# Kernel tuning notes

Hardware: AMD Instinct MI355X
Metric: run time of the kernel (lower is better)

The kernel has to match this reference:

```python
import jax, jax.numpy as jnp
import numpy as np

B = 64
L_IN = 4001
L_CONV = 998  # (4001-10)//4 + 1
D = 1000
EPS = 1e-5


def _convlin(x, cw, cb, lw, lb):
    # x: (B,1,4001), cw: (1,1,10), lw: (1000,998)
    y = jax.lax.conv_general_dilated(
        x, cw, window_strides=(4,), padding='VALID',
        dimension_numbers=('NCH', 'OIH', 'NCH')) + cb[None, :, None]  # (B,1,998)
    y = y @ lw.T + lb  # (B,1,1000)
    return jax.nn.relu(y)


def setup_inputs() -> dict:
    key = jax.random.key(0)
    ks = jax.random.split(key, 24)
    f32 = jnp.float32
    inp = {
        'x': jax.random.normal(ks[0], (B, 1, L_IN), dtype=f32),
        'bn_gamma': jnp.ones((L_IN,), f32),
        'bn_beta': jnp.zeros((L_IN,), f32),
        'bn_mean': jax.random.normal(ks[1], (L_IN,), f32) * 0.1,
        'bn_var': jax.random.uniform(ks[2], (L_IN,), f32, 0.5, 1.5),
        'conv_w_q': jax.random.normal(ks[3], (1, 1, 10), f32) * 0.3,
        'conv_b_q': jax.random.normal(ks[4], (1,), f32) * 0.1,
        'lin_w_q': jax.random.normal(ks[5], (D, L_CONV), f32) * (1.0 / np.sqrt(L_CONV)),
        'lin_b_q': jax.random.normal(ks[6], (D,), f32) * 0.02,
        'conv_w_k': jax.random.normal(ks[7], (1, 1, 10), f32) * 0.3,
        'conv_b_k': jax.random.normal(ks[8], (1,), f32) * 0.1,
        'lin_w_k': jax.random.normal(ks[9], (D, L_CONV), f32) * (1.0 / np.sqrt(L_CONV)),
        'lin_b_k': jax.random.normal(ks[10], (D,), f32) * 0.02,
        'conv_w_v': jax.random.normal(ks[11], (1, 1, 10), f32) * 0.3,
        'conv_b_v': jax.random.normal(ks[12], (1,), f32) * 0.1,
        'lin_w_v': jax.random.normal(ks[13], (D, L_CONV), f32) * (1.0 / np.sqrt(L_CONV)),
        'lin_b_v': jax.random.normal(ks[14], (D,), f32) * 0.02,
        'in_proj_w': jax.random.normal(ks[15], (3, 1), f32),
        'in_proj_b': jax.random.normal(ks[16], (3,), f32) * 0.02,
        'out_proj_w': jax.random.normal(ks[17], (1, 1), f32),
        'out_proj_b': jax.random.normal(ks[18], (1,), f32) * 0.02,
        'out_w': jax.random.normal(ks[19], (D, D), f32) * (1.0 / np.sqrt(D)),
        'out_b': jax.random.normal(ks[20], (D,), f32) * 0.02,
    }
    return inp


def reference(x, bn_gamma, bn_beta, bn_mean, bn_var,
              conv_w_q, conv_b_q, lin_w_q, lin_b_q,
              conv_w_k, conv_b_k, lin_w_k, lin_b_k,
              conv_w_v, conv_b_v, lin_w_v, lin_b_v,
              in_proj_w, in_proj_b, out_proj_w, out_proj_b,
              out_w, out_b):
    # BatchNorm1d over last dim (eval mode, running stats); x: (B,1,4001)
    xn = (x - bn_mean[None, None, :]) * jax.lax.rsqrt(bn_var[None, None, :] + EPS)
    xn = xn * bn_gamma[None, None, :] + bn_beta[None, None, :]

    Q = _convlin(xn, conv_w_q, conv_b_q, lin_w_q, lin_b_q)[:, 0, :]  # (B,1000)
    K = _convlin(xn, conv_w_k, conv_b_k, lin_w_k, lin_b_k)[:, 0, :]
    V = _convlin(xn, conv_w_v, conv_b_v, lin_w_v, lin_b_v)[:, 0, :]

    # MHA with embed_dim=1, num_heads=1 -> scalar in-projections, scale = 1
    q = Q * in_proj_w[0, 0] + in_proj_b[0]  # (B,1000)
    k = K * in_proj_w[1, 0] + in_proj_b[1]
    v = V * in_proj_w[2, 0] + in_proj_b[2]

    scores = q[:, :, None] * k[:, None, :]  # (B,1000,1000)
    attn = jax.nn.softmax(scores, axis=-1)
    ctx = jnp.einsum('bqk,bk->bq', attn, v)  # (B,1000)
    ctx = ctx * out_proj_w[0, 0] + out_proj_b[0]

    out = ctx[:, None, :] @ out_w.T + out_b  # (B,1,1000)
    return out
```

## Files before the change

kernel.cpp:

```cpp
#include <hip/hip_runtime.h>
#include <math.h>

#define NB 64
#define LIN 4001
#define LC 998
#define ND 1000
#define EPSBN 1e-5f

#define CKL 100
#define NCHL 10
#define CKO 50
#define NCHO 20

#define OFF_CONVT 0u
#define OFF_PP    191616u
#define OFF_Q     2157696u
#define OFF_KV    2221696u
#define OFF_CF    2352768u
#define OFF_OP    2416768u

__global__ __launch_bounds__(256) void k_bnconv(
    const float* __restrict__ x,
    const float* __restrict__ g, const float* __restrict__ be,
    const float* __restrict__ mu, const float* __restrict__ va,
    const float* __restrict__ cwq, const float* __restrict__ cbq,
    const float* __restrict__ cwk, const float* __restrict__ cbk,
    const float* __restrict__ cwv, const float* __restrict__ cbv,
    float* __restrict__ convT)
{
    int j = blockIdx.x * 256 + threadIdx.x;
    int b = blockIdx.y;
    if (j >= LC) return;
    const float* xb = x + (size_t)b * LIN + 4 * j;
    float aq = 0.f, ak = 0.f, av = 0.f;
#pragma unroll
    for (int t = 0; t < 10; ++t) {
        int i = 4 * j + t;
        float s  = g[i] * rsqrtf(va[i] + EPSBN);
        float xn = (xb[t] - mu[i]) * s + be[i];
        aq = fmaf(xn, cwq[t], aq);
        ak = fmaf(xn, cwk[t], ak);
        av = fmaf(xn, cwv[t], av);
    }
    convT[((size_t)0 * LC + j) * 64 + b] = aq + cbq[0];
    convT[((size_t)1 * LC + j) * 64 + b] = ak + cbk[0];
    convT[((size_t)2 * LC + j) * 64 + b] = av + cbv[0];
}

template <int CKT>
__device__ __forceinline__ void gemm_tile(
    const float* __restrict__ Asrc,
    const float* __restrict__ Brow,
    int ldB, int dgb, int j0, int jc,
    float* __restrict__ Pt,
    float* lds)
{
    constexpr int LDW = CKT + 1;
    constexpr int F2R = CKT / 2;
    float* ldsC = lds;
    float* ldsW = lds + CKT * 64;
    int tid  = threadIdx.x;
    int lane = tid & 63;
    int w    = tid >> 6;
    int b0   = (lane & 7) << 3;
    int d0   = (lane >> 3) << 3;

    {
        const float4* src = (const float4*)Asrc;
        float4* dst = (float4*)ldsC;
        int n = jc * 16;
        for (int t = tid; t < n; t += 256) dst[t] = src[t];
    }
    for (int idx = tid; idx < 64 * F2R; idx += 256) {
        int dd = idx / F2R, j2 = idx % F2R;
        int dg = dgb + dd;
        float2 v = make_float2(0.f, 0.f);
        if (dg < ND && 2 * j2 < jc)
            v = *(const float2*)(Brow + (size_t)dg * ldB + j0 + 2 * j2);
        ldsW[dd * LDW + 2 * j2]     = v.x;
        ldsW[dd * LDW + 2 * j2 + 1] = v.y;
    }
    __syncthreads();

    float acc[8][8];
#pragma unroll
    for (int i = 0; i < 8; ++i)
#pragma unroll
        for (int jx = 0; jx < 8; ++jx) acc[i][jx] = 0.f;

    int js = (jc * w) >> 2;
    int je = (jc * (w + 1)) >> 2;
    for (int jj = js; jj < je; ++jj) {
        float4 c0 = *(const float4*)(ldsC + jj * 64 + b0);
        float4 c1 = *(const float4*)(ldsC + jj * 64 + b0 + 4);
        float cv[8] = {c0.x, c0.y, c0.z, c0.w, c1.x, c1.y, c1.z, c1.w};
        float wv[8];
#pragma unroll
        for (int r = 0; r < 8; ++r) wv[r] = ldsW[(d0 + r) * LDW + jj];
#pragma unroll
        for (int i = 0; i < 8; ++i)
#pragma unroll
            for (int jx = 0; jx < 8; ++jx)
                acc[i][jx] = fmaf(cv[i], wv[jx], acc[i][jx]);
    }
    __syncthreads();

    for (int p = 0; p < 2; ++p) {
        float* red = lds + w * 2304;
#pragma unroll
        for (int i = 0; i < 8; ++i)
            *(float4*)(red + (b0 + i) * 36 + (d0 >> 1)) =
                make_float4(acc[i][4*p], acc[i][4*p+1], acc[i][4*p+2], acc[i][4*p+3]);
        __syncthreads();
        for (int t = tid; t < 512; t += 256) {
            int bb = t >> 3, gg = t & 7;
            int o = bb * 36 + 4 * gg;
            float4 a0 = *(const float4*)(lds + o);
            float4 a1 = *(const float4*)(lds + 2304 + o);
            float4 a2 = *(const float4*)(lds + 4608 + o);
            float4 a3 = *(const float4*)(lds + 6912 + o);
            float4 s;
            s.x = a0.x + a1.x + a2.x + a3.x;
            s.y = a0.y + a1.y + a2.y + a3.y;
            s.z = a0.z + a1.z + a2.z + a3.z;
            s.w = a0.w + a1.w + a2.w + a3.w;
            *(float4*)(Pt + bb * 64 + 8 * gg + 4 * p) = s;
        }
        __syncthreads();
    }
}

__global__ __launch_bounds__(256) void k_lin(
    const float* __restrict__ convT,
    const float* __restrict__ lwq, const float* __restrict__ lwk,
    const float* __restrict__ lwv,
    float* __restrict__ Pp)
{
    __shared__ float lds[12864];
    int dgb   = blockIdx.x * 64;
    int which = blockIdx.y;
    int chunk = blockIdx.z;
    int j0 = chunk * CKL;
    int jc = (LC - j0 < CKL) ? (LC - j0) : CKL;
    const float* lw = (which == 0) ? lwq : ((which == 1) ? lwk : lwv);
    const float* Asrc = convT + ((size_t)which * LC + j0) * 64;
    float* Pt = Pp + (((size_t)chunk * 3 + which) * 16 + blockIdx.x) * 4096;
    gemm_tile<CKL>(Asrc, lw, LC, dgb, j0, jc, Pt, lds);
}

__global__ __launch_bounds__(256) void k_act(
    const float* __restrict__ Pp,
    const float* __restrict__ lbq, const float* __restrict__ lbk,
    const float* __restrict__ lbv,
    const float* __restrict__ ipw, const float* __restrict__ ipb,
    float* __restrict__ q, float* __restrict__ kv)
{
    int i = blockIdx.x * 256 + threadIdx.x;
    int b = blockIdx.y;
    if (i >= ND) return;
    int it = i >> 6, il = i & 63;
    float s0 = 0.f, s1 = 0.f, s2 = 0.f;
    for (int c = 0; c < NCHL; ++c) {
        size_t base = (((size_t)c * 3) * 16 + it) * 4096 + (il | (b << 6));
        s0 += Pp[base];
        s1 += Pp[base + 16 * 4096];
        s2 += Pp[base + 32 * 4096];
    }
    float yq = fmaxf(s0 + lbq[i], 0.f) * ipw[0] + ipb[0];
    float yk = fmaxf(s1 + lbk[i], 0.f) * ipw[1] + ipb[1];
    float yv = fmaxf(s2 + lbv[i], 0.f) * ipw[2] + ipb[2];
    q[(size_t)b * ND + i] = yq;
    kv[(size_t)b * 2048 + 2 * i]     = yk;
    kv[(size_t)b * 2048 + 2 * i + 1] = yv;
}

__global__ __launch_bounds__(256) void k_attn(
    const float* __restrict__ q, const float* __restrict__ kv,
    const float* __restrict__ opw, const float* __restrict__ opb,
    float* __restrict__ cfT)
{
    __shared__ float ldsKV[2048];
    __shared__ float sden[256];
    __shared__ float snum[256];
    __shared__ float rmax[4];
    __shared__ float rmin[4];
    int tid = threadIdx.x;
    int b   = blockIdx.y;
    int w   = tid >> 6;
    int ii  = tid & 63;
    int i   = blockIdx.x * 64 + ii;

    {
        const float4* src = (const float4*)(kv + (size_t)b * 2048);
        float4* dst = (float4*)ldsKV;
        for (int t = tid; t < 512; t += 256) dst[t] = src[t];
    }
    __syncthreads();

    const float2* kv2 = (const float2*)ldsKV;
    float km = -INFINITY, kn = INFINITY;
    for (int idx = tid; idx < ND; idx += 256) {
        float2 f = kv2[idx];
        km = fmaxf(km, f.x);
        kn = fminf(kn, f.x);
    }
#pragma unroll
    for (int off = 1; off < 64; off <<= 1) {
        km = fmaxf(km, __shfl_xor(km, off));
        kn = fminf(kn, __shfl_xor(kn, off));
    }
    if (ii == 0) { rmax[w] = km; rmin[w] = kn; }
    __syncthreads();
    km = fmaxf(fmaxf(rmax[0], rmax[1]), fmaxf(rmax[2], rmax[3]));
    kn = fminf(fminf(rmin[0], rmin[1]), fminf(rmin[2], rmin[3]));

    float qi = (i < ND) ? q[(size_t)b * ND + i] : 0.f;
    float m  = (qi >= 0.f) ? qi * km : qi * kn;

    int jb = w * 250;
    float den = 0.f, num = 0.f;
#pragma unroll 2
    for (int jl = 0; jl < 250; ++jl) {
        float2 f = kv2[jb + jl];
        float e  = __expf(fmaf(qi, f.x, -m));
        den += e;
        num = fmaf(e, f.y, num);
    }
    sden[tid] = den;
    snum[tid] = num;
    __syncthreads();
    if (w == 0 && i < ND) {
        float dt = sden[ii] + sden[64 + ii] + sden[128 + ii] + sden[192 + ii];
        float nt = snum[ii] + snum[64 + ii] + snum[128 + ii] + snum[192 + ii];
        cfT[(size_t)i * 64 + b] = (nt / dt) * opw[0] + opb[0];
    }
}

__global__ __launch_bounds__(256) void k_out(
    const float* __restrict__ cfT, const float* __restrict__ W,
    float* __restrict__ Op)
{
    __shared__ float lds[9216];
    int egb   = blockIdx.x * 64;
    int chunk = blockIdx.y;
    int j0 = chunk * CKO;
    int jc = (ND - j0 < CKO) ? (ND - j0) : CKO;
    const float* Asrc = cfT + (size_t)j0 * 64;
    float* Pt = Op + ((size_t)chunk * 16 + blockIdx.x) * 4096;
    gemm_tile<CKO>(Asrc, W, ND, egb, j0, jc, Pt, lds);
}

__global__ __launch_bounds__(256) void k_fin(
    const float* __restrict__ Op, const float* __restrict__ outb,
    float* __restrict__ out)
{
    int e = blockIdx.x * 256 + threadIdx.x;
    int b = blockIdx.y;
    if (e >= ND) return;
    float s = outb[e];
    size_t cell = ((size_t)(e >> 6)) * 4096 + (b << 6) + (e & 63);
    for (int c = 0; c < NCHO; ++c)
        s += Op[(size_t)c * 16 * 4096 + cell];
    out[(size_t)b * ND + e] = s;
}

extern "C" void kernel_launch(void* const* d_in, const int* in_sizes, int n_in,
                              void* d_out, int out_size, void* d_ws, size_t ws_size,
                              hipStream_t stream)
{
    const float* x    = (const float*)d_in[0];
    const float* g    = (const float*)d_in[1];
    const float* be   = (const float*)d_in[2];
    const float* mu   = (const float*)d_in[3];
    const float* va   = (const float*)d_in[4];
    const float* cwq  = (const float*)d_in[5];
    const float* cbq  = (const float*)d_in[6];
    const float* lwq  = (const float*)d_in[7];
    const float* lbq  = (const float*)d_in[8];
    const float* cwk  = (const float*)d_in[9];
    const float* cbk  = (const float*)d_in[10];
    const float* lwk  = (const float*)d_in[11];
    const float* lbk  = (const float*)d_in[12];
    const float* cwv  = (const float*)d_in[13];
    const float* cbv  = (const float*)d_in[14];
    const float* lwv  = (const float*)d_in[15];
    const float* lbv  = (const float*)d_in[16];
    const float* ipw  = (const float*)d_in[17];
    const float* ipb  = (const float*)d_in[18];
    const float* opw  = (const float*)d_in[19];
    const float* opb  = (const float*)d_in[20];
    const float* W    = (const float*)d_in[21];
    const float* outb = (const float*)d_in[22];

    float* ws    = (float*)d_ws;
    float* convT = ws + OFF_CONVT;
    float* Pp    = ws + OFF_PP;
    float* q     = ws + OFF_Q;
    float* kv    = ws + OFF_KV;
    float* cfT   = ws + OFF_CF;
    float* Op    = ws + OFF_OP;
    float* out   = (float*)d_out;

    k_bnconv<<<dim3(4, 64), 256, 0, stream>>>(x, g, be, mu, va,
                                              cwq, cbq, cwk, cbk, cwv, cbv, convT);
    k_lin  <<<dim3(16, 3, NCHL), 256, 0, stream>>>(convT, lwq, lwk, lwv, Pp);
    k_act  <<<dim3(4, 64), 256, 0, stream>>>(Pp, lbq, lbk, lbv, ipw, ipb, q, kv);
    k_attn <<<dim3(16, 64), 256, 0, stream>>>(q, kv, opw, opb, cfT);
    k_out  <<<dim3(16, NCHO), 256, 0, stream>>>(cfT, W, Op);
    k_fin  <<<dim3(4, 64), 256, 0, stream>>>(Op, outb, out);
}
```

Before: 168.5 us.

## Fuse BN+conv into linear GEMM kernel and split-K reduction into attention kernel

The separate batchnorm/conv kernel is removed. Each k_lin block now recomputes the conv outputs for its j-chunk directly from x into LDS, and also stages the weight tile itself. The split-K partial reduction, ReLU and in-projection (formerly k_act) move into the start of k_attn, so the q/kv buffers and two launches disappear. The trade-off is redundant conv recomputation across the 16 d-tiles and redundant Pp reduction across the 16 attention blocks per batch.

```diff
diff --git a/kernel.cpp b/kernel.cpp
--- a/kernel.cpp
+++ b/kernel.cpp
@@ -12,40 +12,9 @@
 #define CKO 50
 #define NCHO 20
 
-#define OFF_CONVT 0u
-#define OFF_PP    191616u
-#define OFF_Q     2157696u
-#define OFF_KV    2221696u
-#define OFF_CF    2352768u
-#define OFF_OP    2416768u
-
-__global__ __launch_bounds__(256) void k_bnconv(
-    const float* __restrict__ x,
-    const float* __restrict__ g, const float* __restrict__ be,
-    const float* __restrict__ mu, const float* __restrict__ va,
-    const float* __restrict__ cwq, const float* __restrict__ cbq,
-    const float* __restrict__ cwk, const float* __restrict__ cbk,
-    const float* __restrict__ cwv, const float* __restrict__ cbv,
-    float* __restrict__ convT)
-{
-    int j = blockIdx.x * 256 + threadIdx.x;
-    int b = blockIdx.y;
-    if (j >= LC) return;
-    const float* xb = x + (size_t)b * LIN + 4 * j;
-    float aq = 0.f, ak = 0.f, av = 0.f;
-#pragma unroll
-    for (int t = 0; t < 10; ++t) {
-        int i = 4 * j + t;
-        float s  = g[i] * rsqrtf(va[i] + EPSBN);
-        float xn = (xb[t] - mu[i]) * s + be[i];
-        aq = fmaf(xn, cwq[t], aq);
-        ak = fmaf(xn, cwk[t], ak);
-        av = fmaf(xn, cwv[t], av);
-    }
-    convT[((size_t)0 * LC + j) * 64 + b] = aq + cbq[0];
-    convT[((size_t)1 * LC + j) * 64 + b] = ak + cbk[0];
-    convT[((size_t)2 * LC + j) * 64 + b] = av + cbv[0];
-}
+#define OFF_PP    0u
+#define OFF_CF    1966080u
+#define OFF_OP    2030080u
 
 template <int CKT>
 __device__ __forceinline__ void gemm_tile(
@@ -131,51 +100,128 @@
 }
 
 __global__ __launch_bounds__(256) void k_lin(
-    const float* __restrict__ convT,
+    const float* __restrict__ x,
+    const float* __restrict__ g, const float* __restrict__ be,
+    const float* __restrict__ mu, const float* __restrict__ va,
+    const float* __restrict__ cwq, const float* __restrict__ cbq,
+    const float* __restrict__ cwk, const float* __restrict__ cbk,
+    const float* __restrict__ cwv, const float* __restrict__ cbv,
     const float* __restrict__ lwq, const float* __restrict__ lwk,
     const float* __restrict__ lwv,
     float* __restrict__ Pp)
 {
-    __shared__ float lds[12864];
+    __shared__ float lds[13676];
+    float* ldsC = lds;
+    float* ldsW = lds + 6400;
+    float2* bn2 = (float2*)(lds + 12864);
+
+    int tid   = threadIdx.x;
     int dgb   = blockIdx.x * 64;
     int which = blockIdx.y;
     int chunk = blockIdx.z;
     int j0 = chunk * CKL;
     int jc = (LC - j0 < CKL) ? (LC - j0) : CKL;
     const float* lw = (which == 0) ? lwq : ((which == 1) ? lwk : lwv);
-    const float* Asrc = convT + ((size_t)which * LC + j0) * 64;
+    const float* cw = (which == 0) ? cwq : ((which == 1) ? cwk : cwv);
+    const float* cb = (which == 0) ? cbq : ((which == 1) ? cbk : cbv);
     float* Pt = Pp + (((size_t)chunk * 3 + which) * 16 + blockIdx.x) * 4096;
-    gemm_tile<CKL>(Asrc, lw, LC, dgb, j0, jc, Pt, lds);
-}
-
-__global__ __launch_bounds__(256) void k_act(
+
+    int NI = 4 * jc + 6;
+    for (int idx = tid; idx < NI; idx += 256) {
+        int i = 4 * j0 + idx;
+        float sc = g[i] * rsqrtf(va[i] + EPSBN);
+        bn2[idx] = make_float2(sc, be[i] - mu[i] * sc);
+    }
+    for (int idx = tid; idx < 3200; idx += 256) {
+        int dd = idx / 50, j2 = idx % 50;
+        int dg = dgb + dd;
+        float2 v = make_float2(0.f, 0.f);
+        if (dg < ND && 2 * j2 < jc)
+            v = *(const float2*)(lw + (size_t)dg * LC + j0 + 2 * j2);
+        ldsW[dd * 101 + 2 * j2]     = v.x;
+        ldsW[dd * 101 + 2 * j2 + 1] = v.y;
+    }
+    __syncthreads();
+
+    {
+        int w    = tid >> 6;
+        int b    = tid & 63;
+        float cw_r[10];
+#pragma unroll
+        for (int t = 0; t < 10; ++t) cw_r[t] = cw[t];
+        float cb_r = cb[0];
+        const float* xb = x + (size_t)b * LIN + 4 * j0;
+        for (int jj = w; jj < jc; jj += 4) {
+            float a = cb_r;
+#pragma unroll
+            for (int t = 0; t < 10; ++t) {
+                float2 bnv = bn2[4 * jj + t];
+                float  xn  = fmaf(xb[4 * jj + t], bnv.x, bnv.y);
+                a = fmaf(xn, cw_r[t], a);
+            }
+            ldsC[jj * 64 + b] = a;
+        }
+    }
+    __syncthreads();
+
+    int lane = tid & 63;
+    int w    = tid >> 6;
+    int b0   = (lane & 7) << 3;
+    int d0   = (lane >> 3) << 3;
+
+    float acc[8][8];
+#pragma unroll
+    for (int i = 0; i < 8; ++i)
+#pragma unroll
+        for (int jx = 0; jx < 8; ++jx) acc[i][jx] = 0.f;
+
+    int js = (jc * w) >> 2;
+    int je = (jc * (w + 1)) >> 2;
+    for (int jj = js; jj < je; ++jj) {
+        float4 c0 = *(const float4*)(ldsC + jj * 64 + b0);
+        float4 c1 = *(const float4*)(ldsC + jj * 64 + b0 + 4);
+        float cv[8] = {c0.x, c0.y, c0.z, c0.w, c1.x, c1.y, c1.z, c1.w};
+        float wv[8];
+#pragma unroll
+        for (int r = 0; r < 8; ++r) wv[r] = ldsW[(d0 + r) * 101 + jj];
+#pragma unroll
+        for (int i = 0; i < 8; ++i)
+#pragma unroll
+            for (int jx = 0; jx < 8; ++jx)
+                acc[i][jx] = fmaf(cv[i], wv[jx], acc[i][jx]);
+    }
+    __syncthreads();
+
+    for (int p = 0; p < 2; ++p) {
+        float* red = lds + w * 2304;
+#pragma unroll
+        for (int i = 0; i < 8; ++i)
+            *(float4*)(red + (b0 + i) * 36 + (d0 >> 1)) =
+                make_float4(acc[i][4*p], acc[i][4*p+1], acc[i][4*p+2], acc[i][4*p+3]);
+        __syncthreads();
+        for (int t = tid; t < 512; t += 256) {
+            int bb = t >> 3, gg = t & 7;
+            int o = bb * 36 + 4 * gg;
+            float4 a0 = *(const float4*)(lds + o);
+            float4 a1 = *(const float4*)(lds + 2304 + o);
+            float4 a2 = *(const float4*)(lds + 4608 + o);
+            float4 a3 = *(const float4*)(lds + 6912 + o);
+            float4 s;
+            s.x = a0.x + a1.x + a2.x + a3.x;
+            s.y = a0.y + a1.y + a2.y + a3.y;
+            s.z = a0.z + a1.z + a2.z + a3.z;
+            s.w = a0.w + a1.w + a2.w + a3.w;
+            *(float4*)(Pt + bb * 64 + 8 * gg + 4 * p) = s;
+        }
+        __syncthreads();
+    }
+}
+
+__global__ __launch_bounds__(256) void k_attn(
     const float* __restrict__ Pp,
     const float* __restrict__ lbq, const float* __restrict__ lbk,
     const float* __restrict__ lbv,
     const float* __restrict__ ipw, const float* __restrict__ ipb,
-    float* __restrict__ q, float* __restrict__ kv)
-{
-    int i = blockIdx.x * 256 + threadIdx.x;
-    int b = blockIdx.y;
-    if (i >= ND) return;
-    int it = i >> 6, il = i & 63;
-    float s0 = 0.f, s1 = 0.f, s2 = 0.f;
-    for (int c = 0; c < NCHL; ++c) {
-        size_t base = (((size_t)c * 3) * 16 + it) * 4096 + (il | (b << 6));
-        s0 += Pp[base];
-        s1 += Pp[base + 16 * 4096];
-        s2 += Pp[base + 32 * 4096];
-    }
-    float yq = fmaxf(s0 + lbq[i], 0.f) * ipw[0] + ipb[0];
-    float yk = fmaxf(s1 + lbk[i], 0.f) * ipw[1] + ipb[1];
-    float yv = fmaxf(s2 + lbv[i], 0.f) * ipw[2] + ipb[2];
-    q[(size_t)b * ND + i] = yq;
-    kv[(size_t)b * 2048 + 2 * i]     = yk;
-    kv[(size_t)b * 2048 + 2 * i + 1] = yv;
-}
-
-__global__ __launch_bounds__(256) void k_attn(
-    const float* __restrict__ q, const float* __restrict__ kv,
     const float* __restrict__ opw, const float* __restrict__ opb,
     float* __restrict__ cfT)
 {
@@ -191,9 +237,28 @@
     int i   = blockIdx.x * 64 + ii;
 
     {
-        const float4* src = (const float4*)(kv + (size_t)b * 2048);
-        float4* dst = (float4*)ldsKV;
-        for (int t = tid; t < 512; t += 256) dst[t] = src[t];
+        float w1 = ipw[1], b1 = ipb[1], w2 = ipw[2], b2 = ipb[2];
+        for (int t = tid; t < ND; t += 256) {
+            int ig  = t >> 6;
+            int off = (t & 63) | (b << 6);
+            float s1 = 0.f, s2 = 0.f;
+#pragma unroll
+            for (int c = 0; c < NCHL; ++c) {
+                size_t base = (((size_t)c * 3 + 1) * 16 + ig) * 4096 + off;
+                s1 += Pp[base];
+                s2 += Pp[base + 16 * 4096];
+            }
+            ldsKV[2 * t]     = fmaf(fmaxf(s1 + lbk[t], 0.f), w1, b1);
+            ldsKV[2 * t + 1] = fmaf(fmaxf(s2 + lbv[t], 0.f), w2, b2);
+        }
+    }
+    float qi = 0.f;
+    if (i < ND) {
+        float s0 = 0.f;
+#pragma unroll
+        for (int c = 0; c < NCHL; ++c)
+            s0 += Pp[(((size_t)c * 3) * 16 + blockIdx.x) * 4096 + (ii | (b << 6))];
+        qi = fmaf(fmaxf(s0 + lbq[i], 0.f), ipw[0], ipb[0]);
     }
     __syncthreads();
 
@@ -214,8 +279,7 @@
     km = fmaxf(fmaxf(rmax[0], rmax[1]), fmaxf(rmax[2], rmax[3]));
     kn = fminf(fminf(rmin[0], rmin[1]), fminf(rmin[2], rmin[3]));
 
-    float qi = (i < ND) ? q[(size_t)b * ND + i] : 0.f;
-    float m  = (qi >= 0.f) ? qi * km : qi * kn;
+    float m = (qi >= 0.f) ? qi * km : qi * kn;
 
     int jb = w * 250;
     float den = 0.f, num = 0.f;
@@ -292,20 +356,17 @@
     const float* W    = (const float*)d_in[21];
     const float* outb = (const float*)d_in[22];
 
-    float* ws    = (float*)d_ws;
-    float* convT = ws + OFF_CONVT;
-    float* Pp    = ws + OFF_PP;
-    float* q     = ws + OFF_Q;
-    float* kv    = ws + OFF_KV;
-    float* cfT   = ws + OFF_CF;
-    float* Op    = ws + OFF_OP;
-    float* out   = (float*)d_out;
-
-    k_bnconv<<<dim3(4, 64), 256, 0, stream>>>(x, g, be, mu, va,
-                                              cwq, cbq, cwk, cbk, cwv, cbv, convT);
-    k_lin  <<<dim3(16, 3, NCHL), 256, 0, stream>>>(convT, lwq, lwk, lwv, Pp);
-    k_act  <<<dim3(4, 64), 256, 0, stream>>>(Pp, lbq, lbk, lbv, ipw, ipb, q, kv);
-    k_attn <<<dim3(16, 64), 256, 0, stream>>>(q, kv, opw, opb, cfT);
-    k_out  <<<dim3(16, NCHO), 256, 0, stream>>>(cfT, W, Op);
-    k_fin  <<<dim3(4, 64), 256, 0, stream>>>(Op, outb, out);
-}
+    float* ws  = (float*)d_ws;
+    float* Pp  = ws + OFF_PP;
+    float* cfT = ws + OFF_CF;
+    float* Op  = ws + OFF_OP;
+    float* out = (float*)d_out;
+
+    k_lin <<<dim3(16, 3, NCHL), 256, 0, stream>>>(x, g, be, mu, va,
+                                                  cwq, cbq, cwk, cbk, cwv, cbv,
+                                                  lwq, lwk, lwv, Pp);
+    k_attn<<<dim3(16, 64), 256, 0, stream>>>(Pp, lbq, lbk, lbv,
+                                             ipw, ipb, opw, opb, cfT);
+    k_out <<<dim3(16, NCHO), 256, 0, stream>>>(cfT, W, Op);
+    k_fin <<<dim3(4, 64), 256, 0, stream>>>(Op, outb, out);
+}
```

Measured after the change: 197.0 us. +16.9%, slower.
